# Performance work log

Measured on AMD Instinct MI355X. Metric: run time of the kernel, lower is better.

The kernel has to match this reference:

```python
import jax, jax.numpy as jnp
import numpy as np

N = 8192
D = 1024
TIME_DECAY = 86400.0
EPS = 1e-10


def setup_inputs() -> dict:
    key = jax.random.key(0)
    ks = jax.random.split(key, 8)
    x = jax.random.normal(ks[0], (N, D), dtype=jnp.float32)
    # timestamps spanning ~10 days so decay bias is non-trivial
    timestamps = jax.random.uniform(ks[1], (N,), dtype=jnp.float32) * (10.0 * TIME_DECAY)
    s = 1.0 / np.sqrt(D)
    Wq = jax.random.normal(ks[2], (D, D), dtype=jnp.float32) * s
    bq = jnp.zeros((D,), dtype=jnp.float32)
    Wk = jax.random.normal(ks[3], (D, D), dtype=jnp.float32) * s
    bk = jnp.zeros((D,), dtype=jnp.float32)
    Wv = jax.random.normal(ks[4], (D, D), dtype=jnp.float32) * s
    bv = jnp.zeros((D,), dtype=jnp.float32)
    return {"x": x, "timestamps": timestamps, "Wq": Wq, "bq": bq,
            "Wk": Wk, "bk": bk, "Wv": Wv, "bv": bv}


def reference(x, timestamps, Wq, bq, Wk, bk, Wv, bv):
    scale = jnp.asarray(D ** 0.5, x.dtype)
    # torch nn.Linear: y = x @ W.T + b
    Q = x @ Wq.T + bq          # [N, D]
    K = x @ Wk.T + bk          # [N, D]
    V = x @ Wv.T + bv          # [N, D]
    time_diff = timestamps[:, None] - timestamps[None, :]   # [N, N]
    time_decay = jnp.exp(-jnp.abs(time_diff) / TIME_DECAY)  # [N, N]
    scores = (Q @ K.T) / scale + jnp.log(time_decay + EPS)  # [N, N]
    attn = jax.nn.softmax(scores, axis=-1)
    return attn @ V
```

## Files before the change

kernel.cpp:

```cpp
#include <hip/hip_runtime.h>


using half8   = __attribute__((ext_vector_type(8))) _Float16;
using half4   = __attribute__((ext_vector_type(4))) _Float16;
using floatx4 = __attribute__((ext_vector_type(4))) float;

__device__ __forceinline__ void gload_lds16(const void* g, void* l) {
  __builtin_amdgcn_global_load_lds((const __attribute__((address_space(1))) void*)g,
                                   (__attribute__((address_space(3))) void*)l,
                                   16, 0, 0);
}

template<int N> __device__ __forceinline__ void waitv() {
  if constexpr (N == 6) asm volatile("s_waitcnt vmcnt(6)" ::: "memory");
  else                  asm volatile("s_waitcnt vmcnt(0)" ::: "memory");
}

template<int BM, int BN, int WM, int WN, int SLOTS, int PH, int MI, int NJ>
__device__ __forceinline__ void kloop_f(
    const _Float16* __restrict__ A, const _Float16* __restrict__ B,
    long rowBase, long colBase, int lda, int ldb, int K,
    _Float16* __restrict__ As, _Float16* __restrict__ Bs,
    floatx4 (&acc)[MI][NJ])
{
  static_assert(MI == BM / WM / 16 && NJ == BN / WN / 16 && MI % PH == 0);
  constexpr int LA = BM / 64, LB = BN / 64;
  constexpr int RP = MI / PH;
  const int tid = threadIdx.x;
  const int w = tid >> 6, lane = tid & 63;
  const int q = lane >> 4, l15 = lane & 15;
  const int wr = w / WN, wcn = w & (WN - 1);

  const int sc = ((lane & 7) ^ (lane >> 3)) << 3;
  const _Float16* Agp[LA]; const _Float16* Bgp[LB];
#pragma unroll
  for (int p = 0; p < LA; ++p)
    Agp[p] = A + (rowBase + p * 64 + (tid >> 3)) * (long)lda + sc;
#pragma unroll
  for (int p = 0; p < LB; ++p)
    Bgp[p] = B + (colBase + p * 64 + (tid >> 3)) * (long)ldb + sc;
  const int ldsOff = tid * 8;

  const int aRow = wr * (BM / WM) + l15;
  const int bRow = wcn * (BN / WN) + l15;
  const int cx = l15 & 7;

  auto issueA = [&](int t, int s) {
    _Float16* Asl = As + s * (BM * 64);
    const int ko = t << 6;
#pragma unroll
    for (int p = 0; p < LA; ++p) gload_lds16(Agp[p] + ko, Asl + p * 4096 + ldsOff);
  };
  auto issueB = [&](int t, int s) {
    _Float16* Bsl = Bs + s * (BN * 64);
    const int ko = t << 6;
#pragma unroll
    for (int p = 0; p < LB; ++p) gload_lds16(Bgp[p] + ko, Bsl + p * 4096 + ldsOff);
  };

  half8 bfr[2][NJ];

  auto tile = [&](int t, int slot, bool doStage, int ew) {
    const _Float16* Asl = As + slot * (BM * 64);
    const _Float16* Bsl = Bs + slot * (BN * 64);
    const int st = t + SLOTS - 1;
    const int ss = (SLOTS == 2) ? (slot ^ 1) : (st % 3);
#pragma unroll
    for (int ph = 0; ph < PH; ++ph) {
      half8 afr[2][RP];
      if (ph == 0) {
#pragma unroll
        for (int kk = 0; kk < 2; ++kk) {
          const int pc = ((kk * 4 + q) ^ cx) << 3;
#pragma unroll
          for (int j = 0; j < NJ; ++j)
            bfr[kk][j] = *(const half8*)&Bsl[(bRow + 16 * j) * 64 + pc];
        }
      }
#pragma unroll
      for (int kk = 0; kk < 2; ++kk) {
        const int pc = ((kk * 4 + q) ^ cx) << 3;
#pragma unroll
        for (int r = 0; r < RP; ++r)
          afr[kk][r] = *(const half8*)&Asl[(aRow + 16 * (ph * RP + r)) * 64 + pc];
      }
      if (doStage && ph == 0) issueA(st, ss);
      if (doStage && ph == 1) issueB(st, ss);
      __builtin_amdgcn_s_barrier();
      asm volatile("s_waitcnt lgkmcnt(0)" ::: "memory");
      __builtin_amdgcn_sched_barrier(0);
      __builtin_amdgcn_s_setprio(1);
#pragma unroll
      for (int kk = 0; kk < 2; ++kk)
#pragma unroll
        for (int r = 0; r < RP; ++r)
#pragma unroll
          for (int j = 0; j < NJ; ++j)
            acc[ph * RP + r][j] = __builtin_amdgcn_mfma_f32_16x16x32_f16(
                afr[kk][r], bfr[kk][j], acc[ph * RP + r][j], 0, 0, 0);
      __builtin_amdgcn_s_setprio(0);
      if (ph == PH - 1) {
        if (ew == 6)      waitv<6>();
        else if (ew == 0) waitv<0>();
        if (ew >= 0) __builtin_amdgcn_s_barrier();
      } else {
        __builtin_amdgcn_s_barrier();
      }
    }
  };

  const int NT = K >> 6;
  if constexpr (SLOTS == 2) {
    issueA(0, 0); issueB(0, 0);
    waitv<0>(); __builtin_amdgcn_s_barrier();
    int cs = 0;
    for (int t = 0; t < NT - 1; ++t) {
      tile(t, cs, true, 0);
      cs ^= 1;
    }
    tile(NT - 1, cs, false, -1);
  } else {
    static_assert(SLOTS == 3);
    issueA(0, 0); issueB(0, 0);
    issueA(1, 1); issueB(1, 1);
    waitv<6>(); __builtin_amdgcn_s_barrier();
    int cs = 0;
    for (int t = 0; t < NT - 1; ++t) {
      const bool st = (t + 2 < NT);
      tile(t, cs, st, (t < NT - 2) ? 6 : 0);
      cs = (cs == 2) ? 0 : cs + 1;
    }
    tile(NT - 1, cs, false, -1);
  }
}

template<int BM, int BN, int WM, int WN, int SLOTS, int PH,
         int BIAS_MODE, int OUT_MODE, int SWZ>
__global__ __launch_bounds__(512, 2)
void gemm256_k(const _Float16* __restrict__ A, const _Float16* __restrict__ B,
               void* __restrict__ Cout, const float* __restrict__ bias,
               int lda, int ldb, int ldc, int K, float outScale)
{
  constexpr int MI = BM / WM / 16, NJ = BN / WN / 16;
  __shared__ __align__(16) _Float16 As[SLOTS * BM * 64];
  __shared__ __align__(16) _Float16 Bs[SLOTS * BN * 64];

  int tx, ty;
  if (SWZ) {
    const int bflat = blockIdx.y * gridDim.x + blockIdx.x;
    ty = bflat % gridDim.y;
    tx = bflat / gridDim.y;
  } else {
    tx = blockIdx.x; ty = blockIdx.y;
  }
  const long rowBase = (long)ty * BM;
  const long colBase = (long)tx * BN;

  floatx4 acc[MI][NJ] = {};
  kloop_f<BM, BN, WM, WN, SLOTS, PH, MI, NJ>(A, B, rowBase, colBase, lda, ldb, K,
                                             As, Bs, acc);

  const int tid = threadIdx.x;
  const int w = tid >> 6, lane = tid & 63;
  const int q = lane >> 4, l15 = lane & 15;
  const int wr = w / WN, wcn = w & (WN - 1);
#pragma unroll
  for (int i = 0; i < MI; ++i) {
#pragma unroll
    for (int r = 0; r < 4; ++r) {
      const long rowg = rowBase + wr * (BM / WM) + 16 * i + q * 4 + r;
#pragma unroll
      for (int j = 0; j < NJ; ++j) {
        const long colg = colBase + wcn * (BN / WN) + 16 * j + l15;
        float v = acc[i][j][r];
        if (BIAS_MODE == 1) v += bias[colg];
        if (BIAS_MODE == 2) v += bias[rowg];
        if (BIAS_MODE == 3) v *= bias[rowg];
        v *= outScale;
        if (OUT_MODE == 2) ((float*)Cout)[rowg * ldc + colg] = v;
        else               ((_Float16*)Cout)[rowg * ldc + colg] = (_Float16)v;
      }
    }
  }
}

__global__ __launch_bounds__(512, 2)
void gemm_stats256_k(const _Float16* __restrict__ A, const _Float16* __restrict__ B,
                     const float* __restrict__ ts, _Float16* __restrict__ U,
                     float* __restrict__ part, int lda, int ldb, int N, int K,
                     float qkScale)
{
  constexpr int BM = 256, BN = 256, WM = 2, WN = 4, MI = 8, NJ = 4;
  __shared__ __align__(16) _Float16 As[2 * BM * 64];
  __shared__ __align__(16) _Float16 Bs[2 * BN * 64];
  __shared__ float trs[256], tcs[256];
  __shared__ float sL[2][4][128];
  const int tid = threadIdx.x;
  const long rowBase = (long)blockIdx.y * 256;
  const long colBase = (long)blockIdx.x * 256;

  if (tid < 256) {
    trs[tid] = ts[rowBase + tid];
    tcs[tid] = ts[colBase + tid];
  }

  floatx4 acc[MI][NJ] = {};
  kloop_f<BM, BN, WM, WN, 2, 4, MI, NJ>(A, B, rowBase, colBase, lda, ldb, K,
                                        As, Bs, acc);

  const int w = tid >> 6, lane = tid & 63;
  const int q = lane >> 4, l15 = lane & 15;
  const int wr = w >> 2, wcn = w & 3;
  const float inv_td = 1.0f / 86400.0f;
#pragma unroll
  for (int i = 0; i < 8; ++i) {
#pragma unroll
    for (int r = 0; r < 4; ++r) {
      const int rowl = wr * 128 + 16 * i + q * 4 + r;
      const float tr = trs[rowl];
      float ls = 0.0f;
#pragma unroll
      for (int j = 0; j < 4; ++j) {
        const int coll = wcn * 64 + 16 * j + l15;
        const float sv = acc[i][j][r] * qkScale
                       - fabsf(tr - tcs[coll]) * inv_td - 4.0f;
        const float u = __expf(sv);
        ls += u;
        U[(rowBase + rowl) * (long)N + (colBase + coll)] = (_Float16)u;
      }
      for (int mask = 1; mask <= 8; mask <<= 1)
        ls += __shfl_xor(ls, mask, 64);
      if (l15 == 0) sL[wr][wcn][16 * i + 4 * q + r] = ls;
    }
  }
  __syncthreads();
  if (tid < 256) {
    const int wr2 = tid >> 7, rl = tid & 127;
    part[(rowBase + tid) * 32 + blockIdx.x] =
        sL[wr2][0][rl] + sL[wr2][1][rl] + sL[wr2][2][rl] + sL[wr2][3][rl];
  }
}

__global__ void combine_k(const float* __restrict__ part, float* __restrict__ invL) {
  const int r = blockIdx.x * 256 + threadIdx.x;
  float L = 0.0f;
  for (int c = 0; c < 32; ++c) L += part[(long)r * 32 + c];
  invL[r] = 1.0f / L;
}

__global__ void cvt_k(const float* __restrict__ in, _Float16* __restrict__ out, int n) {
  const int i = (blockIdx.x * 256 + threadIdx.x) * 4;
  if (i >= n) return;
  const float4 v = *(const float4*)(in + i);
  half4 o = { (_Float16)v.x, (_Float16)v.y, (_Float16)v.z, (_Float16)v.w };
  *(half4*)(out + i) = o;
}

extern "C" void kernel_launch(void* const* d_in, const int* in_sizes, int n_in,
                              void* d_out, int out_size, void* d_ws, size_t ws_size,
                              hipStream_t stream)
{
  (void)in_sizes; (void)n_in; (void)out_size; (void)ws_size;
  const int N = 8192, D = 1024;
  const float* x  = (const float*)d_in[0];
  const float* ts = (const float*)d_in[1];
  const float* Wq = (const float*)d_in[2];
  const float* bq = (const float*)d_in[3];
  const float* Wk = (const float*)d_in[4];
  const float* bk = (const float*)d_in[5];
  const float* Wv = (const float*)d_in[6];
  const float* bv = (const float*)d_in[7];

  char* p = (char*)d_ws;
  auto grab = [&](size_t bytes) {
    char* r = p;
    p += (bytes + 255) & ~(size_t)255;
    return r;
  };
  _Float16* xh    = (_Float16*)grab((size_t)N * D * 2);
  _Float16* wqkh  = (_Float16*)grab((size_t)2 * D * D * 2);
  _Float16* wvh   = (_Float16*)grab((size_t)D * D * 2);
  _Float16* QKcat = (_Float16*)grab((size_t)N * 2 * D * 2);
  _Float16* VTh   = (_Float16*)grab((size_t)D * N * 2);
  _Float16* Uh    = (_Float16*)grab((size_t)N * N * 2);
  float*    part  = (float*)grab((size_t)N * 32 * sizeof(float));
  float*    invL  = (float*)grab((size_t)N * sizeof(float));
  float*    bcat  = (float*)grab((size_t)2 * D * sizeof(float));

  cvt_k<<<N * D / 1024, 256, 0, stream>>>(x,  xh,  N * D);
  cvt_k<<<D * D / 1024, 256, 0, stream>>>(Wq, wqkh,         D * D);
  cvt_k<<<D * D / 1024, 256, 0, stream>>>(Wk, wqkh + D * D, D * D);
  cvt_k<<<D * D / 1024, 256, 0, stream>>>(Wv, wvh, D * D);
  hipMemcpyAsync(bcat,     bq, D * sizeof(float), hipMemcpyDeviceToDevice, stream);
  hipMemcpyAsync(bcat + D, bk, D * sizeof(float), hipMemcpyDeviceToDevice, stream);

  dim3 blk(512);
  gemm256_k<256, 256, 2, 4, 2, 4, 1, 0, 0><<<dim3(2 * D / 256, N / 256), blk, 0, stream>>>(
      xh, wqkh, QKcat, bcat, D, D, 2 * D, D, 1.0f);
  gemm256_k<256, 128, 4, 2, 3, 2, 2, 0, 0><<<dim3(N / 128, D / 256), blk, 0, stream>>>(
      wvh, xh, VTh, bv, D, D, N, D, 1.0f);
  gemm_stats256_k<<<dim3(N / 256, N / 256), blk, 0, stream>>>(
      QKcat, QKcat + D, ts, Uh, part, 2 * D, 2 * D, N, D, 1.0f / 32.0f);
  combine_k<<<N / 256, 256, 0, stream>>>(part, invL);
  gemm256_k<256, 128, 4, 2, 3, 2, 3, 2, 1><<<dim3(D / 128, N / 256), blk, 0, stream>>>(
      Uh, VTh, d_out, invL, N, N, D, N, 1.0f);
}
```

Baseline: 487.0 us.

## Add fine-grained staged K-loop with asymmetric LDS buffering for 256x256 GEMMs

Adds a new main loop for 256x256 tiles. It keeps two A slots and three B slots in LDS and splits each K tile into four MFMA quarters, with global-to-LDS loads for the next tiles interleaved between them. This is meant to overlap memory traffic with MFMA work better than the previous two-slot, four-phase loop in the QK projection and the large score GEMM. The stats kernel now reads timestamps straight from global memory and reuses the A buffer for row-sum reduction, which frees LDS for the extra B slot. The risks are more barriers per tile and higher LDS use, which could cut occupancy below two blocks per CU.

```diff
diff --git a/kernel.cpp b/kernel.cpp
--- a/kernel.cpp
+++ b/kernel.cpp
@@ -14,6 +14,129 @@
 template<int N> __device__ __forceinline__ void waitv() {
   if constexpr (N == 6) asm volatile("s_waitcnt vmcnt(6)" ::: "memory");
   else                  asm volatile("s_waitcnt vmcnt(0)" ::: "memory");
+}
+
+template<int MI, int NJ>
+__device__ __forceinline__ void kloop_c(
+    const _Float16* __restrict__ A, const _Float16* __restrict__ B,
+    long rowBase, long colBase, int lda, int ldb, int K,
+    _Float16* __restrict__ As, _Float16* __restrict__ Bs,
+    floatx4 (&acc)[MI][NJ])
+{
+  static_assert(MI == 8 && NJ == 4);
+  const int tid = threadIdx.x;
+  const int w = tid >> 6, lane = tid & 63;
+  const int q = lane >> 4, l15 = lane & 15;
+  const int wr = w >> 2, wcn = w & 3;
+
+  const int sc = ((lane & 7) ^ (lane >> 3)) << 3;
+  const _Float16* Agp[4]; const _Float16* Bgp[4];
+#pragma unroll
+  for (int p = 0; p < 4; ++p) {
+    Agp[p] = A + (rowBase + p * 64 + (tid >> 3)) * (long)lda + sc;
+    Bgp[p] = B + (colBase + p * 64 + (tid >> 3)) * (long)ldb + sc;
+  }
+  const int ldsOff = tid * 8;
+
+  const int aRow = wr * 128 + l15;
+  const int bRow = wcn * 64 + l15;
+  const int cx = l15 & 7;
+  const int pc0 = (q ^ cx) << 3, pc1 = ((4 + q) ^ cx) << 3;
+
+  auto stageA = [&](int t, int h) {
+    _Float16* dst = As + (t & 1) * (256 * 64);
+    const int ko = t << 6;
+#pragma unroll
+    for (int p = 2 * h; p < 2 * h + 2; ++p)
+      gload_lds16(Agp[p] + ko, dst + p * 4096 + ldsOff);
+  };
+  auto stageB = [&](int t, int h, int slot) {
+    _Float16* dst = Bs + slot * (256 * 64);
+    const int ko = t << 6;
+#pragma unroll
+    for (int p = 2 * h; p < 2 * h + 2; ++p)
+      gload_lds16(Bgp[p] + ko, dst + p * 4096 + ldsOff);
+  };
+
+  const int NT = K >> 6;
+  stageB(0, 0, 0); stageB(0, 1, 0); stageA(0, 0); stageA(0, 1);
+  stageB(1, 0, 1); stageB(1, 1, 1); stageA(1, 0);
+  waitv<6>(); __builtin_amdgcn_s_barrier();
+
+  int bs_ = 0;
+  for (int t = 0; t < NT; ++t) {
+    const _Float16* Asl = As + (t & 1) * (256 * 64);
+    const _Float16* Bsl = Bs + bs_ * (256 * 64);
+    const int bs2 = (bs_ == 0) ? 2 : bs_ - 1;
+    half8 b0[NJ], b1[NJ], a0lo[MI / 2], a0hi[MI / 2], a1[MI];
+
+#pragma unroll
+    for (int j = 0; j < NJ; ++j)
+      b0[j] = *(const half8*)&Bsl[(bRow + 16 * j) * 64 + pc0];
+#pragma unroll
+    for (int i = 0; i < MI / 2; ++i)
+      a0lo[i] = *(const half8*)&Asl[(aRow + 16 * i) * 64 + pc0];
+    if (t + 1 < NT) stageA(t + 1, 1);
+    __builtin_amdgcn_s_barrier();
+    asm volatile("s_waitcnt lgkmcnt(0)" ::: "memory");
+    __builtin_amdgcn_sched_barrier(0);
+    __builtin_amdgcn_s_setprio(1);
+#pragma unroll
+    for (int i = 0; i < MI / 2; ++i)
+#pragma unroll
+      for (int j = 0; j < NJ; ++j)
+        acc[i][j] = __builtin_amdgcn_mfma_f32_16x16x32_f16(a0lo[i], b0[j], acc[i][j], 0, 0, 0);
+    __builtin_amdgcn_s_setprio(0);
+    __builtin_amdgcn_s_barrier();
+
+#pragma unroll
+    for (int i = 0; i < MI / 2; ++i)
+      a0hi[i] = *(const half8*)&Asl[(aRow + 16 * (MI / 2 + i)) * 64 + pc0];
+#pragma unroll
+    for (int j = 0; j < NJ; ++j)
+      b1[j] = *(const half8*)&Bsl[(bRow + 16 * j) * 64 + pc1];
+    if (t + 2 < NT) stageB(t + 2, 0, bs2);
+    __builtin_amdgcn_s_barrier();
+    asm volatile("s_waitcnt lgkmcnt(0)" ::: "memory");
+    __builtin_amdgcn_sched_barrier(0);
+    __builtin_amdgcn_s_setprio(1);
+#pragma unroll
+    for (int i = 0; i < MI / 2; ++i)
+#pragma unroll
+      for (int j = 0; j < NJ; ++j)
+        acc[MI / 2 + i][j] = __builtin_amdgcn_mfma_f32_16x16x32_f16(a0hi[i], b0[j], acc[MI / 2 + i][j], 0, 0, 0);
+    __builtin_amdgcn_s_setprio(0);
+    __builtin_amdgcn_s_barrier();
+
+#pragma unroll
+    for (int i = 0; i < MI; ++i)
+      a1[i] = *(const half8*)&Asl[(aRow + 16 * i) * 64 + pc1];
+    if (t + 2 < NT) stageB(t + 2, 1, bs2);
+    __builtin_amdgcn_s_barrier();
+    asm volatile("s_waitcnt lgkmcnt(0)" ::: "memory");
+    __builtin_amdgcn_sched_barrier(0);
+    __builtin_amdgcn_s_setprio(1);
+#pragma unroll
+    for (int i = 0; i < MI / 2; ++i)
+#pragma unroll
+      for (int j = 0; j < NJ; ++j)
+        acc[i][j] = __builtin_amdgcn_mfma_f32_16x16x32_f16(a1[i], b1[j], acc[i][j], 0, 0, 0);
+    __builtin_amdgcn_s_setprio(0);
+    __builtin_amdgcn_s_barrier();
+
+    if (t + 2 < NT) stageA(t + 2, 0);
+    __builtin_amdgcn_s_barrier();
+    __builtin_amdgcn_s_setprio(1);
+#pragma unroll
+    for (int i = 0; i < MI / 2; ++i)
+#pragma unroll
+      for (int j = 0; j < NJ; ++j)
+        acc[MI / 2 + i][j] = __builtin_amdgcn_mfma_f32_16x16x32_f16(a1[MI / 2 + i], b1[j], acc[MI / 2 + i][j], 0, 0, 0);
+    __builtin_amdgcn_s_setprio(0);
+    if (t < NT - 2)       { waitv<6>(); __builtin_amdgcn_s_barrier(); }
+    else if (t == NT - 2) { waitv<0>(); __builtin_amdgcn_s_barrier(); }
+    bs_ = (bs_ == 2) ? 0 : bs_ + 1;
+  }
 }
 
 template<int BM, int BN, int WM, int WN, int SLOTS, int PH, int MI, int NJ>
@@ -110,28 +233,17 @@
   };
 
   const int NT = K >> 6;
-  if constexpr (SLOTS == 2) {
-    issueA(0, 0); issueB(0, 0);
-    waitv<0>(); __builtin_amdgcn_s_barrier();
-    int cs = 0;
-    for (int t = 0; t < NT - 1; ++t) {
-      tile(t, cs, true, 0);
-      cs ^= 1;
-    }
-    tile(NT - 1, cs, false, -1);
-  } else {
-    static_assert(SLOTS == 3);
-    issueA(0, 0); issueB(0, 0);
-    issueA(1, 1); issueB(1, 1);
-    waitv<6>(); __builtin_amdgcn_s_barrier();
-    int cs = 0;
-    for (int t = 0; t < NT - 1; ++t) {
-      const bool st = (t + 2 < NT);
-      tile(t, cs, st, (t < NT - 2) ? 6 : 0);
-      cs = (cs == 2) ? 0 : cs + 1;
-    }
-    tile(NT - 1, cs, false, -1);
-  }
+  static_assert(SLOTS == 3);
+  issueA(0, 0); issueB(0, 0);
+  issueA(1, 1); issueB(1, 1);
+  waitv<6>(); __builtin_amdgcn_s_barrier();
+  int cs = 0;
+  for (int t = 0; t < NT - 1; ++t) {
+    const bool st = (t + 2 < NT);
+    tile(t, cs, st, (t < NT - 2) ? 6 : 0);
+    cs = (cs == 2) ? 0 : cs + 1;
+  }
+  tile(NT - 1, cs, false, -1);
 }
 
 template<int BM, int BN, int WM, int WN, int SLOTS, int PH,
@@ -184,60 +296,96 @@
   }
 }
 
+template<int BIAS_MODE, int OUT_MODE>
 __global__ __launch_bounds__(512, 2)
-void gemm_stats256_k(const _Float16* __restrict__ A, const _Float16* __restrict__ B,
-                     const float* __restrict__ ts, _Float16* __restrict__ U,
-                     float* __restrict__ part, int lda, int ldb, int N, int K,
-                     float qkScale)
-{
-  constexpr int BM = 256, BN = 256, WM = 2, WN = 4, MI = 8, NJ = 4;
-  __shared__ __align__(16) _Float16 As[2 * BM * 64];
-  __shared__ __align__(16) _Float16 Bs[2 * BN * 64];
-  __shared__ float trs[256], tcs[256];
-  __shared__ float sL[2][4][128];
+void gemm256c_k(const _Float16* __restrict__ A, const _Float16* __restrict__ B,
+                void* __restrict__ Cout, const float* __restrict__ bias,
+                int lda, int ldb, int ldc, int K, float outScale)
+{
+  __shared__ __align__(16) _Float16 As[2 * 256 * 64];
+  __shared__ __align__(16) _Float16 Bs[3 * 256 * 64];
+  const long rowBase = (long)blockIdx.y * 256;
+  const long colBase = (long)blockIdx.x * 256;
+
+  floatx4 acc[8][4] = {};
+  kloop_c<8, 4>(A, B, rowBase, colBase, lda, ldb, K, As, Bs, acc);
+
+  const int tid = threadIdx.x;
+  const int w = tid >> 6, lane = tid & 63;
+  const int q = lane >> 4, l15 = lane & 15;
+  const int wr = w >> 2, wcn = w & 3;
+#pragma unroll
+  for (int i = 0; i < 8; ++i) {
+#pragma unroll
+    for (int r = 0; r < 4; ++r) {
+      const long rowg = rowBase + wr * 128 + 16 * i + q * 4 + r;
+#pragma unroll
+      for (int j = 0; j < 4; ++j) {
+        const long colg = colBase + wcn * 64 + 16 * j + l15;
+        float v = acc[i][j][r];
+        if (BIAS_MODE == 1) v += bias[colg];
+        if (BIAS_MODE == 2) v += bias[rowg];
+        v *= outScale;
+        if (OUT_MODE == 2) ((float*)Cout)[rowg * ldc + colg] = v;
+        else               ((_Float16*)Cout)[rowg * ldc + colg] = (_Float16)v;
+      }
+    }
+  }
+}
+
+__global__ __launch_bounds__(512, 2)
+void gemm_statsC_k(const _Float16* __restrict__ A, const _Float16* __restrict__ B,
+                   const float* __restrict__ ts, _Float16* __restrict__ U,
+                   float* __restrict__ part, int lda, int ldb, int N, int K,
+                   float qkScale)
+{
+  __shared__ __align__(16) _Float16 As[2 * 256 * 64];
+  __shared__ __align__(16) _Float16 Bs[3 * 256 * 64];
   const int tid = threadIdx.x;
   const long rowBase = (long)blockIdx.y * 256;
   const long colBase = (long)blockIdx.x * 256;
 
-  if (tid < 256) {
-    trs[tid] = ts[rowBase + tid];
-    tcs[tid] = ts[colBase + tid];
-  }
-
-  floatx4 acc[MI][NJ] = {};
-  kloop_f<BM, BN, WM, WN, 2, 4, MI, NJ>(A, B, rowBase, colBase, lda, ldb, K,
-                                        As, Bs, acc);
+  floatx4 acc[8][4] = {};
+  kloop_c<8, 4>(A, B, rowBase, colBase, lda, ldb, K, As, Bs, acc);
 
   const int w = tid >> 6, lane = tid & 63;
   const int q = lane >> 4, l15 = lane & 15;
   const int wr = w >> 2, wcn = w & 3;
   const float inv_td = 1.0f / 86400.0f;
+
+  float tc[4];
+#pragma unroll
+  for (int j = 0; j < 4; ++j) tc[j] = ts[colBase + wcn * 64 + 16 * j + l15];
+
+  float* sl = (float*)As;
+  __syncthreads();
 #pragma unroll
   for (int i = 0; i < 8; ++i) {
 #pragma unroll
     for (int r = 0; r < 4; ++r) {
       const int rowl = wr * 128 + 16 * i + q * 4 + r;
-      const float tr = trs[rowl];
+      const float tr = ts[rowBase + rowl];
       float ls = 0.0f;
 #pragma unroll
       for (int j = 0; j < 4; ++j) {
         const int coll = wcn * 64 + 16 * j + l15;
         const float sv = acc[i][j][r] * qkScale
-                       - fabsf(tr - tcs[coll]) * inv_td - 4.0f;
+                       - fabsf(tr - tc[j]) * inv_td - 4.0f;
         const float u = __expf(sv);
         ls += u;
         U[(rowBase + rowl) * (long)N + (colBase + coll)] = (_Float16)u;
       }
       for (int mask = 1; mask <= 8; mask <<= 1)
         ls += __shfl_xor(ls, mask, 64);
-      if (l15 == 0) sL[wr][wcn][16 * i + 4 * q + r] = ls;
+      if (l15 == 0) sl[(wr * 4 + wcn) * 128 + 16 * i + 4 * q + r] = ls;
     }
   }
   __syncthreads();
   if (tid < 256) {
-    const int wr2 = tid >> 7, rl = tid & 127;
+    const int band = tid & 127, hi = tid >> 7;
     part[(rowBase + tid) * 32 + blockIdx.x] =
-        sL[wr2][0][rl] + sL[wr2][1][rl] + sL[wr2][2][rl] + sL[wr2][3][rl];
+        sl[(hi * 4 + 0) * 128 + band] + sl[(hi * 4 + 1) * 128 + band] +
+        sl[(hi * 4 + 2) * 128 + band] + sl[(hi * 4 + 3) * 128 + band];
   }
 }
 
@@ -295,11 +443,11 @@
   hipMemcpyAsync(bcat + D, bk, D * sizeof(float), hipMemcpyDeviceToDevice, stream);
 
   dim3 blk(512);
-  gemm256_k<256, 256, 2, 4, 2, 4, 1, 0, 0><<<dim3(2 * D / 256, N / 256), blk, 0, stream>>>(
+  gemm256c_k<1, 0><<<dim3(2 * D / 256, N / 256), blk, 0, stream>>>(
       xh, wqkh, QKcat, bcat, D, D, 2 * D, D, 1.0f);
   gemm256_k<256, 128, 4, 2, 3, 2, 2, 0, 0><<<dim3(N / 128, D / 256), blk, 0, stream>>>(
       wvh, xh, VTh, bv, D, D, N, D, 1.0f);
-  gemm_stats256_k<<<dim3(N / 256, N / 256), blk, 0, stream>>>(
+  gemm_statsC_k<<<dim3(N / 256, N / 256), blk, 0, stream>>>(
       QKcat, QKcat + D, ts, Uh, part, 2 * D, 2 * D, N, D, 1.0f / 32.0f);
   combine_k<<<N / 256, 256, 0, stream>>>(part, invL);
   gemm256_k<256, 128, 4, 2, 3, 2, 3, 2, 1><<<dim3(D / 128, N / 256), blk, 0, stream>>>(
```

Measured after the change: 488.0 us. Within noise of the previous version (+0.2%).
